# Performance work log

Measured on AMD Instinct MI355X. Metric: run time of the kernel, lower is better.

The kernel has to match this reference:

```python
import jax, jax.numpy as jnp
import numpy as np

HIDDEN = 512
IN_FEAT = 512


def setup_inputs() -> dict:
    key = jax.random.key(0)
    ks = jax.random.split(key, 6)
    x = jax.random.normal(ks[0], (128, 1024, IN_FEAT), dtype=jnp.float32)
    # LSTM params: concatenated gates in flax order (i, f, g, o)
    s_in = 1.0 / np.sqrt(IN_FEAT)
    s_h = 1.0 / np.sqrt(HIDDEN)
    Wi = jax.random.normal(ks[1], (IN_FEAT, 4 * HIDDEN), dtype=jnp.float32) * s_in
    Wh = jax.random.normal(ks[2], (HIDDEN, 4 * HIDDEN), dtype=jnp.float32) * s_h
    b = jnp.zeros((4 * HIDDEN,), dtype=jnp.float32)
    Wd = jax.random.normal(ks[3], (HIDDEN, 1), dtype=jnp.float32) * s_h
    bd = jnp.zeros((1,), dtype=jnp.float32)
    return {"x": x, "Wi": Wi, "Wh": Wh, "b": b, "Wd": Wd, "bd": bd}


def reference(x, Wi, Wh, b, Wd, bd):
    B, S, _ = x.shape
    H = Wh.shape[0]
    c0 = jnp.zeros((B, H), dtype=x.dtype)
    h0 = jnp.zeros((B, H), dtype=x.dtype)

    def step(carry, xt):
        c, h = carry
        gates = xt @ Wi + h @ Wh + b  # [B, 4H]
        i, f, g, o = jnp.split(gates, 4, axis=-1)
        c_new = jax.nn.sigmoid(f) * c + jax.nn.sigmoid(i) * jnp.tanh(g)
        h_new = jax.nn.sigmoid(o) * jnp.tanh(c_new)
        return (c_new, h_new), None

    (c_T, h_T), _ = jax.lax.scan(step, (c0, h0), jnp.swapaxes(x, 0, 1))
    # Dense(1) on last timestep output, then squeeze
    return (h_T @ Wd + bd).squeeze(-1)
```

## Files before the change

### kernel.cpp

```cpp
#include <hip/hip_runtime.h>

typedef unsigned int u32;
typedef unsigned short u16;
typedef unsigned long long u64;
typedef float f32x4 __attribute__((ext_vector_type(4)));
typedef _Float16 f16x8 __attribute__((ext_vector_type(8)));
typedef u32 u32x4 __attribute__((ext_vector_type(4)));

#define S_LEN 1024
#define NG 8
#define NM 32
#define GBAT 16
#define PSTR 20

__device__ __forceinline__ u16 f2h_bits(float f) {
  _Float16 h = (_Float16)f;
  return __builtin_bit_cast(u16, h);
}
__device__ __forceinline__ float h2f_bits(u16 b) {
  return (float)__builtin_bit_cast(_Float16, b);
}
__device__ __forceinline__ u32 pk2(float a, float b) {
  return (u32)f2h_bits(a) | ((u32)f2h_bits(b) << 16);
}
__device__ __forceinline__ u32 pkh(u64 v) {
  return (u32)(v & 0xFFFFu) | (((u32)(v >> 32) & 0xFFFFu) << 16);
}

__global__ __launch_bounds__(256) void prep_frags(const float* __restrict__ Wi,
                                                  const float* __restrict__ Wh,
                                                  uint4* __restrict__ wf4,
                                                  u32* __restrict__ det) {
  const int blk = blockIdx.x;
  if (blk == 0) det[threadIdx.x] = 0;
  const int m = blk & 31;
  const float* __restrict__ W = (blk & 32) ? Wh : Wi;
  uint4* __restrict__ dst = wf4 + ((blk & 32) ? 131072 : 0) + m * 4096;
  for (int fi = threadIdx.x; fi < 4096; fi += 256) {
    const int lane = fi & 63;
    const int kc = (fi >> 6) & 15;
    const int q = fi >> 10;
    const int gq = lane >> 4, c = lane & 15;
    const int kb = kc * 32 + gq * 8;
    const int gcol = q * 512 + m * 16 + c;
    u32 wds[4];
#pragma unroll
    for (int pp = 0; pp < 4; ++pp) {
      u16 e0 = f2h_bits(W[(size_t)(kb + 2 * pp) * 2048 + gcol]);
      u16 e1 = f2h_bits(W[(size_t)(kb + 2 * pp + 1) * 2048 + gcol]);
      wds[pp] = (u32)e0 | ((u32)e1 << 16);
    }
    uint4 v; v.x = wds[0]; v.y = wds[1]; v.z = wds[2]; v.w = wds[3];
    dst[fi] = v;
  }
}

__global__ __launch_bounds__(256) void lstm_main(
    const float* __restrict__ x,
    const uint4* __restrict__ wif4,
    u32* __restrict__ hbuf,
    u32* __restrict__ hbuf2,
    u32* __restrict__ det,
    const float* __restrict__ bvec,
    const float* __restrict__ Wd,
    const float* __restrict__ bd,
    float* __restrict__ out) {
  __shared__ __align__(16) uint4 sWi[4096];
  __shared__ __align__(16) uint4 sWh[4096];
  __shared__ __align__(16) float pred[16][PSTR * 16];

  const int tid = threadIdx.x;
  const int lane = tid & 63;
  const int wv = tid >> 6;
  const int g = blockIdx.x & 7;
  const int m = blockIdx.x >> 3;

  for (int i = tid; i < 4096; i += 256) {
    sWi[i] = wif4[m * 4096 + i];
    sWh[i] = wif4[131072 + m * 4096 + i];
  }

  const int bt = tid >> 4;
  const int hi_ = tid & 15;
  const int gb = g * GBAT + bt;
  const int hidx = m * 16 + hi_;

  const float bi = bvec[hidx];
  const float bf_ = bvec[512 + hidx];
  const float bg = bvec[1024 + hidx];
  const float bo = bvec[1536 + hidx];
  float c_reg = 0.f;

  const int abt = lane & 15;
  const int oct = lane >> 4;
  const float* __restrict__ xrow = x + (size_t)(g * GBAT + abt) * (S_LEN * 512);
  const u32 hrow_off = ((u32)(g * GBAT + abt)) << 9;

  __syncthreads();

  bool fastw;
  {
    u32 myxcc;
    asm volatile("s_getreg_b32 %0, hwreg(HW_REG_XCC_ID)" : "=s"(myxcc));
    if (tid == 0)
      __hip_atomic_store(det + g * 32 + m, myxcc + 1u, __ATOMIC_RELAXED,
                         __HIP_MEMORY_SCOPE_AGENT);
    u32 dv;
    for (;;) {
      dv = __hip_atomic_load(det + g * 32 + (lane & 31), __ATOMIC_RELAXED,
                             __HIP_MEMORY_SCOPE_AGENT);
      if (__all(dv != 0u)) break;
      __builtin_amdgcn_s_sleep(1);
    }
    const u32 d0 = __shfl(dv, 0, 64);
    fastw = __all(dv == d0);
  }

  float4 xa[8], xb[8];
#pragma unroll
  for (int kk = 0; kk < 4; ++kk) {
    const int k0 = ((wv << 2) | kk) * 32 + oct * 8;
    xa[2 * kk]     = *reinterpret_cast<const float4*>(xrow + k0);
    xa[2 * kk + 1] = *reinterpret_cast<const float4*>(xrow + k0 + 4);
  }

  auto step = [&](int t, float4* cur, float4* nxt) {
    f32x4 acc0 = {0.f, 0.f, 0.f, 0.f}, acc1 = acc0, acc2 = acc0, acc3 = acc0;
#pragma unroll
    for (int kk = 0; kk < 4; ++kk) {
      const int kc = (wv << 2) | kk;
      uint4 av;
      av.x = pk2(cur[2 * kk].x, cur[2 * kk].y);
      av.y = pk2(cur[2 * kk].z, cur[2 * kk].w);
      av.z = pk2(cur[2 * kk + 1].x, cur[2 * kk + 1].y);
      av.w = pk2(cur[2 * kk + 1].z, cur[2 * kk + 1].w);
      f16x8 af = __builtin_bit_cast(f16x8, av);
      acc0 = __builtin_amdgcn_mfma_f32_16x16x32_f16(af, __builtin_bit_cast(f16x8, sWi[(0 * 16 + kc) * 64 + lane]), acc0, 0, 0, 0);
      acc1 = __builtin_amdgcn_mfma_f32_16x16x32_f16(af, __builtin_bit_cast(f16x8, sWi[(1 * 16 + kc) * 64 + lane]), acc1, 0, 0, 0);
      acc2 = __builtin_amdgcn_mfma_f32_16x16x32_f16(af, __builtin_bit_cast(f16x8, sWi[(2 * 16 + kc) * 64 + lane]), acc2, 0, 0, 0);
      acc3 = __builtin_amdgcn_mfma_f32_16x16x32_f16(af, __builtin_bit_cast(f16x8, sWi[(3 * 16 + kc) * 64 + lane]), acc3, 0, 0, 0);
    }

    if (t > 0) {
      const u32 tg = (u32)t << 16;
      uint4 hv[4];
      bool got = false;

      if (fastw) {
        const u32* p2 = hbuf2 + (((u32)(t & 1)) << 16) + hrow_off +
                        ((u32)((wv << 7) | (oct << 3)));
        int spins = 0;
        for (;;) {
          u32x4 fA0, fB0, fA1, fB1, fA2, fB2, fA3, fB3;
          asm volatile("global_load_dwordx4 %0, %1, off sc0" : "=&v"(fA0) : "v"(p2));
          asm volatile("global_load_dwordx4 %0, %1, off offset:16 sc0" : "=&v"(fB0) : "v"(p2));
          asm volatile("global_load_dwordx4 %0, %1, off offset:128 sc0" : "=&v"(fA1) : "v"(p2));
          asm volatile("global_load_dwordx4 %0, %1, off offset:144 sc0" : "=&v"(fB1) : "v"(p2));
          asm volatile("global_load_dwordx4 %0, %1, off offset:256 sc0" : "=&v"(fA2) : "v"(p2));
          asm volatile("global_load_dwordx4 %0, %1, off offset:272 sc0" : "=&v"(fB2) : "v"(p2));
          asm volatile("global_load_dwordx4 %0, %1, off offset:384 sc0" : "=&v"(fA3) : "v"(p2));
          asm volatile("global_load_dwordx4 %0, %1, off offset:400 sc0" : "=&v"(fB3) : "v"(p2));
          asm volatile("s_waitcnt vmcnt(0)" ::: "memory");
          __builtin_amdgcn_sched_barrier(0);
          u32 bad = (fA0.x ^ tg) | (fA0.y ^ tg) | (fA0.z ^ tg) | (fA0.w ^ tg);
          bad |= (fB0.x ^ tg) | (fB0.y ^ tg) | (fB0.z ^ tg) | (fB0.w ^ tg);
          bad |= (fA1.x ^ tg) | (fA1.y ^ tg) | (fA1.z ^ tg) | (fA1.w ^ tg);
          bad |= (fB1.x ^ tg) | (fB1.y ^ tg) | (fB1.z ^ tg) | (fB1.w ^ tg);
          bad |= (fA2.x ^ tg) | (fA2.y ^ tg) | (fA2.z ^ tg) | (fA2.w ^ tg);
          bad |= (fB2.x ^ tg) | (fB2.y ^ tg) | (fB2.z ^ tg) | (fB2.w ^ tg);
          bad |= (fA3.x ^ tg) | (fA3.y ^ tg) | (fA3.z ^ tg) | (fA3.w ^ tg);
          bad |= (fB3.x ^ tg) | (fB3.y ^ tg) | (fB3.z ^ tg) | (fB3.w ^ tg);
          if (__all((bad & 0xFFFF0000u) == 0u)) {
            hv[0].x = (fA0.x & 0xFFFFu) | (fA0.y << 16); hv[0].y = (fA0.z & 0xFFFFu) | (fA0.w << 16);
            hv[0].z = (fB0.x & 0xFFFFu) | (fB0.y << 16); hv[0].w = (fB0.z & 0xFFFFu) | (fB0.w << 16);
            hv[1].x = (fA1.x & 0xFFFFu) | (fA1.y << 16); hv[1].y = (fA1.z & 0xFFFFu) | (fA1.w << 16);
            hv[1].z = (fB1.x & 0xFFFFu) | (fB1.y << 16); hv[1].w = (fB1.z & 0xFFFFu) | (fB1.w << 16);
            hv[2].x = (fA2.x & 0xFFFFu) | (fA2.y << 16); hv[2].y = (fA2.z & 0xFFFFu) | (fA2.w << 16);
            hv[2].z = (fB2.x & 0xFFFFu) | (fB2.y << 16); hv[2].w = (fB2.z & 0xFFFFu) | (fB2.w << 16);
            hv[3].x = (fA3.x & 0xFFFFu) | (fA3.y << 16); hv[3].y = (fA3.z & 0xFFFFu) | (fA3.w << 16);
            hv[3].z = (fB3.x & 0xFFFFu) | (fB3.y << 16); hv[3].w = (fB3.z & 0xFFFFu) | (fB3.w << 16);
            got = true;
            break;
          }
          if (++spins > 512) { fastw = false; break; }
        }
      }

      if (!got) {
        const u64* hp = reinterpret_cast<const u64*>(hbuf + (u32)(t & 1) * 65536u + hrow_off);
        const u64 wpat = ((u64)tg) | ((u64)tg << 32);
        u64 raw[4][4];
        for (;;) {
#pragma unroll
          for (int kk = 0; kk < 4; ++kk) {
            const int base = (((wv << 2) | kk) << 4) | (oct << 2);
#pragma unroll
            for (int ee = 0; ee < 4; ++ee)
              raw[kk][ee] = __hip_atomic_load(hp + base + ee, __ATOMIC_RELAXED,
                                              __HIP_MEMORY_SCOPE_AGENT);
          }
          __builtin_amdgcn_sched_barrier(0);
          u64 chk = 0;
#pragma unroll
          for (int kk = 0; kk < 4; ++kk)
#pragma unroll
            for (int ee = 0; ee < 4; ++ee)
              chk |= (raw[kk][ee] ^ wpat) & 0xFFFF0000FFFF0000ull;
          if (__all(chk == 0)) break;
          __builtin_amdgcn_s_sleep(1);
        }
#pragma unroll
        for (int kk = 0; kk < 4; ++kk) {
          hv[kk].x = pkh(raw[kk][0]); hv[kk].y = pkh(raw[kk][1]);
          hv[kk].z = pkh(raw[kk][2]); hv[kk].w = pkh(raw[kk][3]);
        }
      }

      {
        int tn = t + 1; tn = (tn < S_LEN) ? tn : (S_LEN - 1);
        const float* xr = xrow + (size_t)tn * 512;
#pragma unroll
        for (int kk = 0; kk < 4; ++kk) {
          const int k0 = ((wv << 2) | kk) * 32 + oct * 8;
          nxt[2 * kk]     = *reinterpret_cast<const float4*>(xr + k0);
          nxt[2 * kk + 1] = *reinterpret_cast<const float4*>(xr + k0 + 4);
        }
      }

#pragma unroll
      for (int kk = 0; kk < 4; ++kk) {
        const int kc = (wv << 2) | kk;
        f16x8 hf = __builtin_bit_cast(f16x8, hv[kk]);
        acc0 = __builtin_amdgcn_mfma_f32_16x16x32_f16(hf, __builtin_bit_cast(f16x8, sWh[(0 * 16 + kc) * 64 + lane]), acc0, 0, 0, 0);
        acc1 = __builtin_amdgcn_mfma_f32_16x16x32_f16(hf, __builtin_bit_cast(f16x8, sWh[(1 * 16 + kc) * 64 + lane]), acc1, 0, 0, 0);
        acc2 = __builtin_amdgcn_mfma_f32_16x16x32_f16(hf, __builtin_bit_cast(f16x8, sWh[(2 * 16 + kc) * 64 + lane]), acc2, 0, 0, 0);
        acc3 = __builtin_amdgcn_mfma_f32_16x16x32_f16(hf, __builtin_bit_cast(f16x8, sWh[(3 * 16 + kc) * 64 + lane]), acc3, 0, 0, 0);
      }
    } else {
      const float* xr = xrow + 512;
#pragma unroll
      for (int kk = 0; kk < 4; ++kk) {
        const int k0 = ((wv << 2) | kk) * 32 + oct * 8;
        nxt[2 * kk]     = *reinterpret_cast<const float4*>(xr + k0);
        nxt[2 * kk + 1] = *reinterpret_cast<const float4*>(xr + k0 + 4);
      }
    }

    {
      const int cc = lane & 15;
      const int r0 = (lane >> 4) << 2;
      *reinterpret_cast<f32x4*>(&pred[wv * 4 + 0][PSTR * cc + r0]) = acc0;
      *reinterpret_cast<f32x4*>(&pred[wv * 4 + 1][PSTR * cc + r0]) = acc1;
      *reinterpret_cast<f32x4*>(&pred[wv * 4 + 2][PSTR * cc + r0]) = acc2;
      *reinterpret_cast<f32x4*>(&pred[wv * 4 + 3][PSTR * cc + r0]) = acc3;
    }
    asm volatile("s_waitcnt lgkmcnt(0)" ::: "memory");
    __builtin_amdgcn_s_barrier();
    __builtin_amdgcn_sched_barrier(0);

    {
      float gi = bi, gf = bf_, gg = bg, go = bo;
#pragma unroll
      for (int w2 = 0; w2 < 4; ++w2) {
        gi += pred[w2 * 4 + 0][PSTR * hi_ + bt];
        gf += pred[w2 * 4 + 1][PSTR * hi_ + bt];
        gg += pred[w2 * 4 + 2][PSTR * hi_ + bt];
        go += pred[w2 * 4 + 3][PSTR * hi_ + bt];
      }
      const float si = 1.f / (1.f + __expf(-gi));
      const float sf = 1.f / (1.f + __expf(-gf));
      const float so = 1.f / (1.f + __expf(-go));
      c_reg = sf * c_reg + si * tanhf(gg);
      const float hv_ = so * tanhf(c_reg);
      const u32 word = ((u32)(t + 1) << 16) | (u32)f2h_bits(hv_);
      const u32 idx = (u32)((t + 1) & 1) * 65536u + (u32)gb * 512u + (u32)hidx;
      *reinterpret_cast<volatile u32*>(hbuf2 + idx) = word;
      __hip_atomic_store(hbuf + idx, word, __ATOMIC_RELAXED,
                         __HIP_MEMORY_SCOPE_AGENT);
    }
    __builtin_amdgcn_s_barrier();
    __builtin_amdgcn_sched_barrier(0);
  };

  for (int t = 0; t < S_LEN; t += 2) {
    step(t, xa, xb);
    step(t + 1, xb, xa);
  }

  if (m == 0) {
    const int btf = tid >> 4;
    const int part = tid & 15;
    const u64* hp = reinterpret_cast<const u64*>(hbuf + (((u32)(g * GBAT + btf)) << 9));
    const u32 want = (u32)S_LEN;
    const u64 wpat = ((u64)want << 16) | ((u64)want << 48);
    u64 rawv[16];
    for (;;) {
#pragma unroll
      for (int j2 = 0; j2 < 16; ++j2)
        rawv[j2] = __hip_atomic_load(hp + part * 16 + j2, __ATOMIC_RELAXED,
                                     __HIP_MEMORY_SCOPE_AGENT);
      __builtin_amdgcn_sched_barrier(0);
      u64 chk = 0;
#pragma unroll
      for (int j2 = 0; j2 < 16; ++j2)
        chk |= (rawv[j2] ^ wpat) & 0xFFFF0000FFFF0000ull;
      if (__all(chk == 0)) break;
      __builtin_amdgcn_s_sleep(1);
    }
    float acc = 0.f;
#pragma unroll
    for (int j2 = 0; j2 < 16; ++j2) {
      const int k = part * 32 + 2 * j2;
      acc += h2f_bits((u16)(rawv[j2] & 0xFFFFu)) * Wd[k] +
             h2f_bits((u16)((rawv[j2] >> 32) & 0xFFFFu)) * Wd[k + 1];
    }
#pragma unroll
    for (int s = 1; s < 16; s <<= 1) acc += __shfl_xor(acc, s, 64);
    if (part == 0) out[g * GBAT + btf] = acc + bd[0];
  }
}

extern "C" void kernel_launch(void* const* d_in, const int* in_sizes, int n_in,
                              void* d_out, int out_size, void* d_ws, size_t ws_size,
                              hipStream_t stream) {
  const float* x = (const float*)d_in[0];
  const float* Wi = (const float*)d_in[1];
  const float* Wh = (const float*)d_in[2];
  const float* bv = (const float*)d_in[3];
  const float* Wd = (const float*)d_in[4];
  const float* bd = (const float*)d_in[5];
  float* out = (float*)d_out;

  char* ws = (char*)d_ws;
  uint4* wif4 = (uint4*)ws;
  u32* hbuf = (u32*)(ws + (4u << 20));
  u32* hbuf2 = (u32*)(ws + (4u << 20) + (512u << 10));
  u32* det = (u32*)(ws + (5u << 20));

  hipLaunchKernelGGL(prep_frags, dim3(64), dim3(256), 0, stream, Wi, Wh, wif4, det);

  const float* kx = x;
  const uint4* kw = wif4;
  u32* kh = hbuf;
  u32* kh2 = hbuf2;
  u32* kd = det;
  const float* kbv = bv;
  const float* kwd = Wd;
  const float* kbd = bd;
  float* ko = out;
  void* args[] = {&kx, &kw, &kh, &kh2, &kd, &kbv, &kwd, &kbd, &ko};
  (void)hipLaunchCooperativeKernel(reinterpret_cast<void*>(lstm_main), dim3(NG * NM),
                                   dim3(256), args, 0, stream);
}
```

Baseline: 4.847 ms.

## Assign batch groups by XCC via atomic roster so recurrent exchange stays XCC-local

New measurement: 3.947 ms (median of 3 runs). 1.23x faster.

```diff
diff --git a/kernel.cpp b/kernel.cpp
--- a/kernel.cpp
+++ b/kernel.cpp
@@ -30,9 +30,9 @@
 __global__ __launch_bounds__(256) void prep_frags(const float* __restrict__ Wi,
                                                   const float* __restrict__ Wh,
                                                   uint4* __restrict__ wf4,
-                                                  u32* __restrict__ det) {
+                                                  u32* __restrict__ roster) {
   const int blk = blockIdx.x;
-  if (blk == 0) det[threadIdx.x] = 0;
+  if (blk == 0 && threadIdx.x < 16) roster[threadIdx.x] = 0;
   const int m = blk & 31;
   const float* __restrict__ W = (blk & 32) ? Wh : Wi;
   uint4* __restrict__ dst = wf4 + ((blk & 32) ? 131072 : 0) + m * 4096;
@@ -59,8 +59,7 @@
     const float* __restrict__ x,
     const uint4* __restrict__ wif4,
     u32* __restrict__ hbuf,
-    u32* __restrict__ hbuf2,
-    u32* __restrict__ det,
+    u32* __restrict__ roster,
     const float* __restrict__ bvec,
     const float* __restrict__ Wd,
     const float* __restrict__ bd,
@@ -68,12 +67,31 @@
   __shared__ __align__(16) uint4 sWi[4096];
   __shared__ __align__(16) uint4 sWh[4096];
   __shared__ __align__(16) float pred[16][PSTR * 16];
+  __shared__ u32 sMode, sG, sM;
 
   const int tid = threadIdx.x;
   const int lane = tid & 63;
   const int wv = tid >> 6;
-  const int g = blockIdx.x & 7;
-  const int m = blockIdx.x >> 3;
+
+  if (tid == 0) {
+    u32 myxcc;
+    asm volatile("s_getreg_b32 %0, hwreg(HW_REG_XCC_ID)" : "=s"(myxcc));
+    const u32 x8 = myxcc & 7u;
+    const u32 slot = __hip_atomic_fetch_add(roster + x8, 1u, __ATOMIC_RELAXED,
+                                            __HIP_MEMORY_SCOPE_AGENT);
+    __hip_atomic_fetch_add(roster + 8, 1u, __ATOMIC_RELAXED, __HIP_MEMORY_SCOPE_AGENT);
+    while (__hip_atomic_load(roster + 8, __ATOMIC_RELAXED, __HIP_MEMORY_SCOPE_AGENT) < 256u)
+      __builtin_amdgcn_s_sleep(1);
+    u32 ok = (slot < 32u) ? 1u : 0u;
+    for (int k = 0; k < 8; ++k)
+      ok &= (__hip_atomic_load(roster + k, __ATOMIC_RELAXED,
+                               __HIP_MEMORY_SCOPE_AGENT) == 32u) ? 1u : 0u;
+    sMode = ok; sG = x8; sM = slot;
+  }
+  __syncthreads();
+  const bool fastm = (sMode != 0u);
+  const int g = fastm ? (int)sG : ((int)blockIdx.x & 7);
+  const int m = fastm ? (int)sM : ((int)blockIdx.x >> 3);
 
   for (int i = tid; i < 4096; i += 256) {
     sWi[i] = wif4[m * 4096 + i];
@@ -98,24 +116,6 @@
 
   __syncthreads();
 
-  bool fastw;
-  {
-    u32 myxcc;
-    asm volatile("s_getreg_b32 %0, hwreg(HW_REG_XCC_ID)" : "=s"(myxcc));
-    if (tid == 0)
-      __hip_atomic_store(det + g * 32 + m, myxcc + 1u, __ATOMIC_RELAXED,
-                         __HIP_MEMORY_SCOPE_AGENT);
-    u32 dv;
-    for (;;) {
-      dv = __hip_atomic_load(det + g * 32 + (lane & 31), __ATOMIC_RELAXED,
-                             __HIP_MEMORY_SCOPE_AGENT);
-      if (__all(dv != 0u)) break;
-      __builtin_amdgcn_s_sleep(1);
-    }
-    const u32 d0 = __shfl(dv, 0, 64);
-    fastw = __all(dv == d0);
-  }
-
   float4 xa[8], xb[8];
 #pragma unroll
   for (int kk = 0; kk < 4; ++kk) {
@@ -125,6 +125,17 @@
   }
 
   auto step = [&](int t, float4* cur, float4* nxt) {
+    {
+      int tn = t + 1; tn = (tn < S_LEN) ? tn : (S_LEN - 1);
+      const float* xr = xrow + (size_t)tn * 512;
+#pragma unroll
+      for (int kk = 0; kk < 4; ++kk) {
+        const int k0 = ((wv << 2) | kk) * 32 + oct * 8;
+        nxt[2 * kk]     = *reinterpret_cast<const float4*>(xr + k0);
+        nxt[2 * kk + 1] = *reinterpret_cast<const float4*>(xr + k0 + 4);
+      }
+    }
+
     f32x4 acc0 = {0.f, 0.f, 0.f, 0.f}, acc1 = acc0, acc2 = acc0, acc3 = acc0;
 #pragma unroll
     for (int kk = 0; kk < 4; ++kk) {
@@ -144,12 +155,10 @@
     if (t > 0) {
       const u32 tg = (u32)t << 16;
       uint4 hv[4];
-      bool got = false;
-
-      if (fastw) {
-        const u32* p2 = hbuf2 + (((u32)(t & 1)) << 16) + hrow_off +
+
+      if (fastm) {
+        const u32* p2 = hbuf + (((u32)(t & 1)) << 16) + hrow_off +
                         ((u32)((wv << 7) | (oct << 3)));
-        int spins = 0;
         for (;;) {
           u32x4 fA0, fB0, fA1, fB1, fA2, fB2, fA3, fB3;
           asm volatile("global_load_dwordx4 %0, %1, off sc0" : "=&v"(fA0) : "v"(p2));
@@ -179,14 +188,11 @@
             hv[2].z = (fB2.x & 0xFFFFu) | (fB2.y << 16); hv[2].w = (fB2.z & 0xFFFFu) | (fB2.w << 16);
             hv[3].x = (fA3.x & 0xFFFFu) | (fA3.y << 16); hv[3].y = (fA3.z & 0xFFFFu) | (fA3.w << 16);
             hv[3].z = (fB3.x & 0xFFFFu) | (fB3.y << 16); hv[3].w = (fB3.z & 0xFFFFu) | (fB3.w << 16);
-            got = true;
             break;
           }
-          if (++spins > 512) { fastw = false; break; }
+          __builtin_amdgcn_s_sleep(1);
         }
-      }
-
-      if (!got) {
+      } else {
         const u64* hp = reinterpret_cast<const u64*>(hbuf + (u32)(t & 1) * 65536u + hrow_off);
         const u64 wpat = ((u64)tg) | ((u64)tg << 32);
         u64 raw[4][4];
@@ -213,17 +219,6 @@
         for (int kk = 0; kk < 4; ++kk) {
           hv[kk].x = pkh(raw[kk][0]); hv[kk].y = pkh(raw[kk][1]);
           hv[kk].z = pkh(raw[kk][2]); hv[kk].w = pkh(raw[kk][3]);
-        }
-      }
-
-      {
-        int tn = t + 1; tn = (tn < S_LEN) ? tn : (S_LEN - 1);
-        const float* xr = xrow + (size_t)tn * 512;
-#pragma unroll
-        for (int kk = 0; kk < 4; ++kk) {
-          const int k0 = ((wv << 2) | kk) * 32 + oct * 8;
-          nxt[2 * kk]     = *reinterpret_cast<const float4*>(xr + k0);
-          nxt[2 * kk + 1] = *reinterpret_cast<const float4*>(xr + k0 + 4);
         }
       }
 
@@ -236,14 +231,6 @@
         acc2 = __builtin_amdgcn_mfma_f32_16x16x32_f16(hf, __builtin_bit_cast(f16x8, sWh[(2 * 16 + kc) * 64 + lane]), acc2, 0, 0, 0);
         acc3 = __builtin_amdgcn_mfma_f32_16x16x32_f16(hf, __builtin_bit_cast(f16x8, sWh[(3 * 16 + kc) * 64 + lane]), acc3, 0, 0, 0);
       }
-    } else {
-      const float* xr = xrow + 512;
-#pragma unroll
-      for (int kk = 0; kk < 4; ++kk) {
-        const int k0 = ((wv << 2) | kk) * 32 + oct * 8;
-        nxt[2 * kk]     = *reinterpret_cast<const float4*>(xr + k0);
-        nxt[2 * kk + 1] = *reinterpret_cast<const float4*>(xr + k0 + 4);
-      }
     }
 
     {
@@ -274,9 +261,10 @@
       const float hv_ = so * tanhf(c_reg);
       const u32 word = ((u32)(t + 1) << 16) | (u32)f2h_bits(hv_);
       const u32 idx = (u32)((t + 1) & 1) * 65536u + (u32)gb * 512u + (u32)hidx;
-      *reinterpret_cast<volatile u32*>(hbuf2 + idx) = word;
-      __hip_atomic_store(hbuf + idx, word, __ATOMIC_RELAXED,
-                         __HIP_MEMORY_SCOPE_AGENT);
+      if (fastm)
+        *reinterpret_cast<volatile u32*>(hbuf + idx) = word;
+      else
+        __hip_atomic_store(hbuf + idx, word, __ATOMIC_RELAXED, __HIP_MEMORY_SCOPE_AGENT);
     }
     __builtin_amdgcn_s_barrier();
     __builtin_amdgcn_sched_barrier(0);
@@ -290,29 +278,65 @@
   if (m == 0) {
     const int btf = tid >> 4;
     const int part = tid & 15;
-    const u64* hp = reinterpret_cast<const u64*>(hbuf + (((u32)(g * GBAT + btf)) << 9));
-    const u32 want = (u32)S_LEN;
-    const u64 wpat = ((u64)want << 16) | ((u64)want << 48);
-    u64 rawv[16];
-    for (;;) {
-#pragma unroll
-      for (int j2 = 0; j2 < 16; ++j2)
-        rawv[j2] = __hip_atomic_load(hp + part * 16 + j2, __ATOMIC_RELAXED,
-                                     __HIP_MEMORY_SCOPE_AGENT);
-      __builtin_amdgcn_sched_barrier(0);
-      u64 chk = 0;
-#pragma unroll
-      for (int j2 = 0; j2 < 16; ++j2)
-        chk |= (rawv[j2] ^ wpat) & 0xFFFF0000FFFF0000ull;
-      if (__all(chk == 0)) break;
-      __builtin_amdgcn_s_sleep(1);
-    }
+    const u32 tg = (u32)S_LEN << 16;
     float acc = 0.f;
-#pragma unroll
-    for (int j2 = 0; j2 < 16; ++j2) {
-      const int k = part * 32 + 2 * j2;
-      acc += h2f_bits((u16)(rawv[j2] & 0xFFFFu)) * Wd[k] +
-             h2f_bits((u16)((rawv[j2] >> 32) & 0xFFFFu)) * Wd[k + 1];
+    if (fastm) {
+      const u32* ep = hbuf + (((u32)(g * GBAT + btf)) << 9) + (u32)part * 32u;
+      u32x4 r0_, r1_, r2_, r3_, r4_, r5_, r6_, r7_;
+      for (;;) {
+        asm volatile("global_load_dwordx4 %0, %1, off sc0" : "=&v"(r0_) : "v"(ep));
+        asm volatile("global_load_dwordx4 %0, %1, off offset:16 sc0" : "=&v"(r1_) : "v"(ep));
+        asm volatile("global_load_dwordx4 %0, %1, off offset:32 sc0" : "=&v"(r2_) : "v"(ep));
+        asm volatile("global_load_dwordx4 %0, %1, off offset:48 sc0" : "=&v"(r3_) : "v"(ep));
+        asm volatile("global_load_dwordx4 %0, %1, off offset:64 sc0" : "=&v"(r4_) : "v"(ep));
+        asm volatile("global_load_dwordx4 %0, %1, off offset:80 sc0" : "=&v"(r5_) : "v"(ep));
+        asm volatile("global_load_dwordx4 %0, %1, off offset:96 sc0" : "=&v"(r6_) : "v"(ep));
+        asm volatile("global_load_dwordx4 %0, %1, off offset:112 sc0" : "=&v"(r7_) : "v"(ep));
+        asm volatile("s_waitcnt vmcnt(0)" ::: "memory");
+        __builtin_amdgcn_sched_barrier(0);
+        u32 bad = (r0_.x ^ tg) | (r0_.y ^ tg) | (r0_.z ^ tg) | (r0_.w ^ tg);
+        bad |= (r1_.x ^ tg) | (r1_.y ^ tg) | (r1_.z ^ tg) | (r1_.w ^ tg);
+        bad |= (r2_.x ^ tg) | (r2_.y ^ tg) | (r2_.z ^ tg) | (r2_.w ^ tg);
+        bad |= (r3_.x ^ tg) | (r3_.y ^ tg) | (r3_.z ^ tg) | (r3_.w ^ tg);
+        bad |= (r4_.x ^ tg) | (r4_.y ^ tg) | (r4_.z ^ tg) | (r4_.w ^ tg);
+        bad |= (r5_.x ^ tg) | (r5_.y ^ tg) | (r5_.z ^ tg) | (r5_.w ^ tg);
+        bad |= (r6_.x ^ tg) | (r6_.y ^ tg) | (r6_.z ^ tg) | (r6_.w ^ tg);
+        bad |= (r7_.x ^ tg) | (r7_.y ^ tg) | (r7_.z ^ tg) | (r7_.w ^ tg);
+        if (__all((bad & 0xFFFF0000u) == 0u)) break;
+        __builtin_amdgcn_s_sleep(1);
+      }
+      const u32x4 rr[8] = {r0_, r1_, r2_, r3_, r4_, r5_, r6_, r7_};
+#pragma unroll
+      for (int j = 0; j < 8; ++j) {
+        const int k = part * 32 + 4 * j;
+        acc += h2f_bits((u16)(rr[j].x & 0xFFFFu)) * Wd[k] +
+               h2f_bits((u16)(rr[j].y & 0xFFFFu)) * Wd[k + 1] +
+               h2f_bits((u16)(rr[j].z & 0xFFFFu)) * Wd[k + 2] +
+               h2f_bits((u16)(rr[j].w & 0xFFFFu)) * Wd[k + 3];
+      }
+    } else {
+      const u64* hp = reinterpret_cast<const u64*>(hbuf + (((u32)(g * GBAT + btf)) << 9));
+      const u64 wpat = ((u64)tg) | ((u64)tg << 32);
+      u64 rawv[16];
+      for (;;) {
+#pragma unroll
+        for (int j2 = 0; j2 < 16; ++j2)
+          rawv[j2] = __hip_atomic_load(hp + part * 16 + j2, __ATOMIC_RELAXED,
+                                       __HIP_MEMORY_SCOPE_AGENT);
+        __builtin_amdgcn_sched_barrier(0);
+        u64 chk = 0;
+#pragma unroll
+        for (int j2 = 0; j2 < 16; ++j2)
+          chk |= (rawv[j2] ^ wpat) & 0xFFFF0000FFFF0000ull;
+        if (__all(chk == 0)) break;
+        __builtin_amdgcn_s_sleep(1);
+      }
+#pragma unroll
+      for (int j2 = 0; j2 < 16; ++j2) {
+        const int k = part * 32 + 2 * j2;
+        acc += h2f_bits((u16)(rawv[j2] & 0xFFFFu)) * Wd[k] +
+               h2f_bits((u16)((rawv[j2] >> 32) & 0xFFFFu)) * Wd[k + 1];
+      }
     }
 #pragma unroll
     for (int s = 1; s < 16; s <<= 1) acc += __shfl_xor(acc, s, 64);
@@ -334,21 +358,19 @@
   char* ws = (char*)d_ws;
   uint4* wif4 = (uint4*)ws;
   u32* hbuf = (u32*)(ws + (4u << 20));
-  u32* hbuf2 = (u32*)(ws + (4u << 20) + (512u << 10));
-  u32* det = (u32*)(ws + (5u << 20));
-
-  hipLaunchKernelGGL(prep_frags, dim3(64), dim3(256), 0, stream, Wi, Wh, wif4, det);
+  u32* roster = (u32*)(ws + (4u << 20) + (512u << 10));
+
+  hipLaunchKernelGGL(prep_frags, dim3(64), dim3(256), 0, stream, Wi, Wh, wif4, roster);
 
   const float* kx = x;
   const uint4* kw = wif4;
   u32* kh = hbuf;
-  u32* kh2 = hbuf2;
-  u32* kd = det;
+  u32* kr = roster;
   const float* kbv = bv;
   const float* kwd = Wd;
   const float* kbd = bd;
   float* ko = out;
-  void* args[] = {&kx, &kw, &kh, &kh2, &kd, &kbv, &kwd, &kbd, &ko};
+  void* args[] = {&kx, &kw, &kh, &kr, &kbv, &kwd, &kbd, &ko};
   (void)hipLaunchCooperativeKernel(reinterpret_cast<void*>(lstm_main), dim3(NG * NM),
                                    dim3(256), args, 0, stream);
 }
```
